# Kernel tuning notes

Measured on AMD Instinct MI355X. Metric: run time of the kernel, lower is better.

## Reference

```python
import math
import jax, jax.numpy as jnp
import numpy as np

B, D, N, KP1 = 64, 128, 500000, 4096  # batch, input_size, output_size, K+1
MOMENTUM = 0.5


def setup_inputs() -> dict:
    key = jax.random.key(0)
    k0, k1, k2, k3, k4, k5 = jax.random.split(key, 6)
    stdv = 1.0 / math.sqrt(D / 3)
    image = jax.random.normal(k0, (B, D), jnp.float32)
    gene = jax.random.normal(k1, (B, D), jnp.float32)
    index = jax.random.randint(k2, (B,), 0, N, dtype=jnp.int32)
    idx = jax.random.randint(k3, (B, KP1), 0, N, dtype=jnp.int32)
    idx = idx.at[:, 0].set(index)  # positive sample in slot 0
    memory_image = jax.random.uniform(k4, (N, D), jnp.float32) * (2 * stdv) - stdv
    memory_gene = jax.random.uniform(k5, (N, D), jnp.float32) * (2 * stdv) - stdv
    return {"image": image, "gene": gene, "memory_image": memory_image,
            "memory_gene": memory_gene, "index": index, "idx": idx}


def _momentum_update(mem, x, index):
    # gather positive rows, momentum blend, L2 normalize, scatter back
    pos = mem[index] * MOMENTUM + x * (1.0 - MOMENTUM)          # [B, D]
    pos = pos / jnp.sqrt(jnp.sum(pos * pos, axis=1, keepdims=True))
    return mem.at[index].set(pos)


def reference(image, gene, memory_image, memory_gene, index, idx):
    # gathered bank rows are detached in the original (weights .detach())
    w_gene = jax.lax.stop_gradient(memory_gene[idx])    # [B, K+1, D]
    w_image = jax.lax.stop_gradient(memory_image[idx])  # [B, K+1, D]
    # bmm([B,K+1,D], [B,D,1]) -> scores [B, K+1]; use_softmax=False branch:
    # stabilized softmax over the K+1 candidates (no temperature division)
    out_image = jax.nn.softmax(jnp.einsum('bkd,bd->bk', w_gene, image), axis=1)
    out_gene = jax.nn.softmax(jnp.einsum('bkd,bd->bk', w_image, gene), axis=1)
    # no_grad momentum scatter-update of the banks
    new_mem_image = _momentum_update(memory_image, jax.lax.stop_gradient(image), index)
    new_mem_gene = _momentum_update(memory_gene, jax.lax.stop_gradient(gene), index)
    return out_image, out_gene, new_mem_image, new_mem_gene
```

## Files before the change

kernel.cpp:

```cpp
#include <hip/hip_runtime.h>
#include <math.h>

constexpr int Bb   = 64;
constexpr int Dd   = 128;
constexpr int KP1  = 4096;
constexpr int Nrow = 500000;
constexpr long NMEM = (long)Nrow * Dd;
constexpr int BK   = Bb * KP1;

constexpr int MSLOT = 16;
constexpr int NGROUP = 31250;
constexpr int GPB    = 15625;
constexpr int SGQ    = 8;
constexpr int NSG    = (NGROUP + SGQ - 1) / SGQ;
constexpr long WS_NEED = (long)Nrow * 4 * (1 + MSLOT);

typedef float f4 __attribute__((ext_vector_type(4)));

__device__ __forceinline__ float dot8(float4 a, float4 b, float4 x0, float4 x1) {
    return a.x*x0.x + a.y*x0.y + a.z*x0.z + a.w*x0.w
         + b.x*x1.x + b.y*x1.y + b.z*x1.z + b.w*x1.w;
}


__global__ __launch_bounds__(512) void zero_cnt(int* cnt) {
    int i = blockIdx.x * 512 + threadIdx.x;
    for (; i < Nrow; i += gridDim.x * 512) cnt[i] = 0;
}

__global__ __launch_bounds__(512) void build_inv(
    const int* __restrict__ idx, int* __restrict__ cnt, int* __restrict__ entries)
{
    const int j = blockIdx.x * 512 + threadIdx.x;
    const int r = idx[j];
    const int c = atomicAdd(&cnt[r], 1);
    if (c < MSLOT) entries[r * MSLOT + c] = j;
}

__global__ __launch_bounds__(512, 2) void copy_score(
    const float* __restrict__ image, const float* __restrict__ gene,
    const float* __restrict__ mem_image, const float* __restrict__ mem_gene,
    const int* __restrict__ cnt, const int* __restrict__ entries,
    float* __restrict__ out)
{
    const int tid  = threadIdx.x;
    const int half = tid >> 5;
    const int lane = tid & 31;

    __shared__ f4  lxi[2048];
    __shared__ f4  lxg[2048];
    __shared__ int scnt[256];
    __shared__ int se0[256];
    {
        const f4* gi = (const f4*)image;
        const f4* gg = (const f4*)gene;
        #pragma unroll
        for (int u = 0; u < 4; ++u) {
            lxi[u * 512 + tid] = gi[u * 512 + tid];
            lxg[u * 512 + tid] = gg[u * 512 + tid];
        }
    }
    __syncthreads();

    const f4* srcI = (const f4*)mem_image;
    const f4* srcG = (const f4*)mem_gene;
    f4* dst = (f4*)(out + 2 * BK);

    for (int G0 = blockIdx.x * SGQ; G0 < NGROUP; G0 += gridDim.x * SGQ) {
        const int gl = (NGROUP - G0 < SGQ) ? (NGROUP - G0) : SGQ;

        f4 v[16];
        #pragma unroll
        for (int q = 0; q < SGQ; ++q) {
            if (q < gl) {
                const int G = G0 + q;
                const f4* s = (G < GPB) ? srcI + (long)G * 1024
                                        : srcG + (long)(G - GPB) * 1024;
                v[2 * q]     = s[tid];
                v[2 * q + 1] = s[512 + tid];
            }
        }
        {
            const int slot = tid & 255;
            const int q    = slot >> 5;
            if (q < gl) {
                const int G   = G0 + q;
                const int row = ((G < GPB) ? G : G - GPB) * 32 + (slot & 31);
                if (tid < 256) scnt[slot] = cnt[row];
                else           se0[slot]  = entries[row * MSLOT];
            }
        }

        #pragma unroll
        for (int q = 0; q < SGQ; ++q) {
            if (q < gl) {
                const long dbase = (long)(G0 + q) * 1024;
                __builtin_nontemporal_store(v[2 * q],     dst + dbase + tid);
                __builtin_nontemporal_store(v[2 * q + 1], dst + dbase + 512 + tid);
            }
        }
        __syncthreads();

        #pragma unroll
        for (int q = 0; q < SGQ; ++q) {
            if (q < gl) {
                const int G     = G0 + q;
                const int bank  = (G >= GPB);
                const int rbase = (bank ? G - GPB : G) * 32;
                const f4* lx    = bank ? lxi : lxg;
                float* odir     = bank ? out : out + BK;
                #pragma unroll
                for (int s2 = 0; s2 < 2; ++s2) {
                    const int slot = q * 32 + s2 * 16 + half;
                    int n = scnt[slot];
                    if (n <= 0) continue;
                    n = (n < MSLOT) ? n : MSLOT;
                    const f4 rv = v[2 * q + s2];
                    int j = se0[slot];
                    for (int e = 0;;) {
                        const f4 xv = lx[(j >> 12) * 32 + lane];
                        float s = rv.x*xv.x + rv.y*xv.y + rv.z*xv.z + rv.w*xv.w;
                        s += __shfl_xor(s, 1);
                        s += __shfl_xor(s, 2);
                        s += __shfl_xor(s, 4);
                        s += __shfl_xor(s, 8);
                        s += __shfl_xor(s, 16);
                        if (lane == 0) odir[j] = s;
                        if (++e >= n) break;
                        j = entries[(rbase + s2 * 16 + half) * MSLOT + e];
                    }
                }
            }
        }
        __syncthreads();
    }
}

__global__ __launch_bounds__(512) void epilogue(
    const float* __restrict__ image, const float* __restrict__ gene,
    const float* __restrict__ mem_image, const float* __restrict__ mem_gene,
    const int* __restrict__ index, float* __restrict__ out)
{
    const int tid = threadIdx.x;

    if (blockIdx.x < 128) {
        f4* row = (f4*)(out + (long)blockIdx.x * KP1);
        __shared__ float red[8];

        f4 a = row[tid], b = row[tid + 512];
        float m = fmaxf(fmaxf(fmaxf(a.x, a.y), fmaxf(a.z, a.w)),
                        fmaxf(fmaxf(b.x, b.y), fmaxf(b.z, b.w)));
        #pragma unroll
        for (int off = 1; off < 64; off <<= 1) m = fmaxf(m, __shfl_xor(m, off));
        if ((tid & 63) == 0) red[tid >> 6] = m;
        __syncthreads();
        if (tid < 64) {
            float tv = (tid < 8) ? red[tid] : -INFINITY;
            #pragma unroll
            for (int off = 1; off < 8; off <<= 1) tv = fmaxf(tv, __shfl_xor(tv, off));
            if (tid == 0) red[0] = tv;
        }
        __syncthreads();
        m = red[0];
        __syncthreads();

        a.x = expf(a.x - m); a.y = expf(a.y - m); a.z = expf(a.z - m); a.w = expf(a.w - m);
        b.x = expf(b.x - m); b.y = expf(b.y - m); b.z = expf(b.z - m); b.w = expf(b.w - m);
        float sum = a.x + a.y + a.z + a.w + b.x + b.y + b.z + b.w;
        #pragma unroll
        for (int off = 1; off < 64; off <<= 1) sum += __shfl_xor(sum, off);
        if ((tid & 63) == 0) red[tid >> 6] = sum;
        __syncthreads();
        if (tid < 64) {
            float tv = (tid < 8) ? red[tid] : 0.f;
            #pragma unroll
            for (int off = 1; off < 8; off <<= 1) tv += __shfl_xor(tv, off);
            if (tid == 0) red[0] = tv;
        }
        __syncthreads();
        const float inv = 1.0f / red[0];
        a *= inv; b *= inv;
        row[tid] = a; row[tid + 512] = b;
        return;
    }

    const int task  = ((blockIdx.x - 128) << 2) | (tid >> 7);
    const int sub   = tid >> 7;
    const int d     = tid & 127;
    const int which = task >> 6;
    const int b     = task & 63;
    const float* mem = which ? mem_gene : mem_image;
    const float* x   = which ? gene : image;
    float* o = out + 2 * BK + (long)which * NMEM;

    const long row = index[b];
    float p = mem[row * Dd + d] * 0.5f + x[(long)b * Dd + d] * 0.5f;
    float ss = p * p;
    #pragma unroll
    for (int off = 1; off < 64; off <<= 1) ss += __shfl_xor(ss, off);
    __shared__ float r2[8];
    if ((tid & 63) == 0) r2[tid >> 6] = ss;
    __syncthreads();
    const float inv = 1.0f / sqrtf(r2[2 * sub] + r2[2 * sub + 1]);
    o[row * Dd + d] = p * inv;
}


constexpr long HALF_F4    = NMEM / 4;
constexpr int  CHUNK_F4   = 8192;
constexpr int  FULL_PER_B = 1953;
constexpr long TAIL_BASE  = (long)FULL_PER_B * CHUNK_F4;
constexpr int  CHUNKS_PER_BANK = FULL_PER_B + 1;
constexpr int  NCHUNK     = 2 * CHUNKS_PER_BANK;

__global__ __launch_bounds__(64) void zero_ctr(unsigned* ctr) {
    if (threadIdx.x == 0) *ctr = 0u;
}

__global__ __launch_bounds__(512, 2) void fused_scores_copy(
    const float* __restrict__ image, const float* __restrict__ gene,
    const float* __restrict__ mem_image, const float* __restrict__ mem_gene,
    const int* __restrict__ idx, float* __restrict__ out, unsigned* __restrict__ ctr)
{
    const int tid = threadIdx.x;

    if (blockIdx.x < 128) {
        const int b     = blockIdx.x >> 1;
        const int which = blockIdx.x & 1;
        const float* w = which ? mem_image : mem_gene;
        const float* x = which ? gene : image;
        float* o = out + (long)which * BK + (long)b * KP1;

        __shared__ int   sidx[KP1];
        __shared__ float sv[KP1];
        __shared__ float red[8];
        {
            const int4* s4 = (const int4*)(idx + (long)b * KP1);
            int4* d4 = (int4*)sidx;
            d4[tid]       = s4[tid];
            d4[tid + 512] = s4[tid + 512];
        }
        const int lg  = tid & 15;
        const int grp = tid >> 4;
        float4 x0 = *(const float4*)(x + b * Dd + lg * 8);
        float4 x1 = *(const float4*)(x + b * Dd + lg * 8 + 4);
        __syncthreads();

        for (int j = 0; j < 128; j += 4) {
            const int k0 = grp + (j + 0) * 32;
            const int k1 = grp + (j + 1) * 32;
            const int k2 = grp + (j + 2) * 32;
            const int k3 = grp + (j + 3) * 32;
            const float4* r0 = (const float4*)(w + (long)sidx[k0] * Dd + lg * 8);
            const float4* r1 = (const float4*)(w + (long)sidx[k1] * Dd + lg * 8);
            const float4* r2 = (const float4*)(w + (long)sidx[k2] * Dd + lg * 8);
            const float4* r3 = (const float4*)(w + (long)sidx[k3] * Dd + lg * 8);
            float4 a0 = r0[0], b0 = r0[1];
            float4 a1 = r1[0], b1 = r1[1];
            float4 a2 = r2[0], b2 = r2[1];
            float4 a3 = r3[0], b3 = r3[1];
            float d0 = dot8(a0, b0, x0, x1);
            float d1 = dot8(a1, b1, x0, x1);
            float d2 = dot8(a2, b2, x0, x1);
            float d3 = dot8(a3, b3, x0, x1);
            d0 += __shfl_xor(d0, 1); d1 += __shfl_xor(d1, 1);
            d2 += __shfl_xor(d2, 1); d3 += __shfl_xor(d3, 1);
            d0 += __shfl_xor(d0, 2); d1 += __shfl_xor(d1, 2);
            d2 += __shfl_xor(d2, 2); d3 += __shfl_xor(d3, 2);
            d0 += __shfl_xor(d0, 4); d1 += __shfl_xor(d1, 4);
            d2 += __shfl_xor(d2, 4); d3 += __shfl_xor(d3, 4);
            d0 += __shfl_xor(d0, 8); d1 += __shfl_xor(d1, 8);
            d2 += __shfl_xor(d2, 8); d3 += __shfl_xor(d3, 8);
            if (lg == 0) { sv[k0] = d0; sv[k1] = d1; sv[k2] = d2; sv[k3] = d3; }
        }
        __syncthreads();

        float m = fmaxf(sv[tid], sv[tid + 512]);
        m = fmaxf(m, fmaxf(sv[tid + 1024], sv[tid + 1536]));
        m = fmaxf(m, fmaxf(sv[tid + 2048], sv[tid + 2560]));
        m = fmaxf(m, fmaxf(sv[tid + 3072], sv[tid + 3584]));
        #pragma unroll
        for (int off = 1; off < 64; off <<= 1) m = fmaxf(m, __shfl_xor(m, off));
        if ((tid & 63) == 0) red[tid >> 6] = m;
        __syncthreads();
        if (tid < 64) {
            float tv = (tid < 8) ? red[tid] : -INFINITY;
            #pragma unroll
            for (int off = 1; off < 8; off <<= 1) tv = fmaxf(tv, __shfl_xor(tv, off));
            if (tid == 0) red[0] = tv;
        }
        __syncthreads();
        m = red[0];
        __syncthreads();

        float sum = 0.f;
        #pragma unroll
        for (int r = 0; r < 8; ++r) {
            int k = tid + r * 512;
            float e = expf(sv[k] - m);
            sv[k] = e;
            sum += e;
        }
        #pragma unroll
        for (int off = 1; off < 64; off <<= 1) sum += __shfl_xor(sum, off);
        if ((tid & 63) == 0) red[tid >> 6] = sum;
        __syncthreads();
        if (tid < 64) {
            float tv = (tid < 8) ? red[tid] : 0.f;
            #pragma unroll
            for (int off = 1; off < 8; off <<= 1) tv += __shfl_xor(tv, off);
            if (tid == 0) red[0] = tv;
        }
        __syncthreads();
        const float inv = 1.0f / red[0];
        #pragma unroll
        for (int r = 0; r < 8; ++r) { int k = tid + r * 512; o[k] = sv[k] * inv; }
    }

    const f4* srcI = (const f4*)mem_image;
    const f4* srcG = (const f4*)mem_gene;
    f4* dst = (f4*)(out + 2 * BK);

    __shared__ unsigned sc;
    for (;;) {
        if (tid == 0) sc = atomicAdd(ctr, 1u);
        __syncthreads();
        const unsigned c = sc;
        __syncthreads();
        if (c >= NCHUNK) break;
        const int  bank  = (c < CHUNKS_PER_BANK) ? 0 : 1;
        const int  local = bank ? (int)(c - CHUNKS_PER_BANK) : (int)c;
        const f4*  sbank = bank ? srcG : srcI;
        const long dbank = (long)bank * HALF_F4;
        if (local < FULL_PER_B) {
            const long base = (long)local * CHUNK_F4;
            f4 v[16];
            #pragma unroll
            for (int k = 0; k < 16; ++k) v[k] = sbank[base + k * 512 + tid];
            #pragma unroll
            for (int k = 0; k < 16; ++k)
                __builtin_nontemporal_store(v[k], dst + dbank + base + k * 512 + tid);
        } else {
            f4 v0 = sbank[TAIL_BASE + tid];
            f4 v1 = sbank[TAIL_BASE + 512 + tid];
            __builtin_nontemporal_store(v0, dst + dbank + TAIL_BASE + tid);
            __builtin_nontemporal_store(v1, dst + dbank + TAIL_BASE + 512 + tid);
        }
    }
}

__global__ __launch_bounds__(128) void momentum_update(
    const float* __restrict__ image, const float* __restrict__ gene,
    const float* __restrict__ mem_image, const float* __restrict__ mem_gene,
    const int* __restrict__ index, float* __restrict__ out)
{
    const int b     = blockIdx.x;
    const int which = blockIdx.y;
    const float* mem = which ? mem_gene : mem_image;
    const float* x   = which ? gene : image;
    float* o = out + 2 * BK + (long)which * NMEM;
    const long row = index[b];
    const int d = threadIdx.x;
    float p = mem[row * Dd + d] * 0.5f + x[(long)b * Dd + d] * 0.5f;
    float ss = p * p;
    #pragma unroll
    for (int off = 1; off < 64; off <<= 1) ss += __shfl_xor(ss, off);
    __shared__ float r2[2];
    if ((d & 63) == 0) r2[d >> 6] = ss;
    __syncthreads();
    const float inv = 1.0f / sqrtf(r2[0] + r2[1]);
    o[row * Dd + d] = p * inv;
}

extern "C" void kernel_launch(void* const* d_in, const int* in_sizes, int n_in,
                              void* d_out, int out_size, void* d_ws, size_t ws_size,
                              hipStream_t stream) {
    const float* image     = (const float*)d_in[0];
    const float* gene      = (const float*)d_in[1];
    const float* mem_image = (const float*)d_in[2];
    const float* mem_gene  = (const float*)d_in[3];
    const int*   index     = (const int*)d_in[4];
    const int*   idx       = (const int*)d_in[5];
    float* out = (float*)d_out;

    if ((long)ws_size >= WS_NEED) {
        int* cnt     = (int*)d_ws;
        int* entries = cnt + Nrow;
        zero_cnt<<<dim3(1024), 512, 0, stream>>>(cnt);
        build_inv<<<dim3(512), 512, 0, stream>>>(idx, cnt, entries);
        copy_score<<<dim3(1954), 512, 0, stream>>>(
            image, gene, mem_image, mem_gene, cnt, entries, out);
        epilogue<<<dim3(160), 512, 0, stream>>>(
            image, gene, mem_image, mem_gene, index, out);
    } else {
        unsigned* ctr = (unsigned*)d_ws;
        zero_ctr<<<dim3(1), 64, 0, stream>>>(ctr);
        fused_scores_copy<<<dim3(2048), 512, 0, stream>>>(
            image, gene, mem_image, mem_gene, idx, out, ctr);
        momentum_update<<<dim3(64, 2), 128, 0, stream>>>(
            image, gene, mem_image, mem_gene, index, out);
    }
}
```

Baseline: 229.1 us.

## Restructure inverted-index copy_score into per-wave group ranges with packed count/first-entry metadata

The inverted index now packs each row's count and first entry into one int2, with overflow entries stored separately, and is cleared with a memset instead of a zeroing kernel. copy_score launches 512 blocks, each fixed to one bank so only that bank's query vectors go into LDS. Each 64-lane wave processes a contiguous range of 32-row groups without block-level barriers. Score dots use 16-lane subgroups that re-read the row from global memory, likely from cache, which trades extra loads for removing __syncthreads and raising occupancy.

```diff
diff --git a/kernel.cpp b/kernel.cpp
--- a/kernel.cpp
+++ b/kernel.cpp
@@ -7,13 +7,15 @@
 constexpr int Nrow = 500000;
 constexpr long NMEM = (long)Nrow * Dd;
 constexpr int BK   = Bb * KP1;
-
-constexpr int MSLOT = 16;
-constexpr int NGROUP = 31250;
-constexpr int GPB    = 15625;
-constexpr int SGQ    = 8;
-constexpr int NSG    = (NGROUP + SGQ - 1) / SGQ;
-constexpr long WS_NEED = (long)Nrow * 4 * (1 + MSLOT);
+constexpr long HALF_F4 = NMEM / 4;
+
+constexpr int GPB  = 15625;
+constexpr int NBLK = 512;
+constexpr int NWB  = (NBLK / 2) * 8;
+constexpr int OVSLOT = 15;
+constexpr long META_B    = (long)Nrow * 8;
+constexpr long ENTRIES_B = (long)Nrow * OVSLOT * 4;
+constexpr long WS_NEED   = META_B + ENTRIES_B;
 
 typedef float f4 __attribute__((ext_vector_type(4)));
 
@@ -23,116 +25,83 @@
 }
 
 
-__global__ __launch_bounds__(512) void zero_cnt(int* cnt) {
-    int i = blockIdx.x * 512 + threadIdx.x;
-    for (; i < Nrow; i += gridDim.x * 512) cnt[i] = 0;
-}
-
 __global__ __launch_bounds__(512) void build_inv(
-    const int* __restrict__ idx, int* __restrict__ cnt, int* __restrict__ entries)
+    const int* __restrict__ idx, int2* __restrict__ meta, int* __restrict__ entries)
 {
     const int j = blockIdx.x * 512 + threadIdx.x;
     const int r = idx[j];
-    const int c = atomicAdd(&cnt[r], 1);
-    if (c < MSLOT) entries[r * MSLOT + c] = j;
-}
-
-__global__ __launch_bounds__(512, 2) void copy_score(
+    const int c = atomicAdd(&meta[r].x, 1);
+    if (c == 0) meta[r].y = j;
+    else if (c <= OVSLOT) entries[(long)r * OVSLOT + (c - 1)] = j;
+}
+
+__global__ __launch_bounds__(512, 4) void copy_score(
     const float* __restrict__ image, const float* __restrict__ gene,
     const float* __restrict__ mem_image, const float* __restrict__ mem_gene,
-    const int* __restrict__ cnt, const int* __restrict__ entries,
+    const int2* __restrict__ meta, const int* __restrict__ entries,
     float* __restrict__ out)
 {
     const int tid  = threadIdx.x;
-    const int half = tid >> 5;
-    const int lane = tid & 31;
-
-    __shared__ f4  lxi[2048];
-    __shared__ f4  lxg[2048];
-    __shared__ int scnt[256];
-    __shared__ int se0[256];
+    const int bank = blockIdx.x & 1;
+    const int wid  = tid >> 6;
+    const int lane = tid & 63;
+    const int lg   = lane & 15;
+    const int sgid = (lane >> 4) & 3;
+
+    __shared__ f4 lx[2048];
     {
-        const f4* gi = (const f4*)image;
-        const f4* gg = (const f4*)gene;
-        #pragma unroll
-        for (int u = 0; u < 4; ++u) {
-            lxi[u * 512 + tid] = gi[u * 512 + tid];
-            lxg[u * 512 + tid] = gg[u * 512 + tid];
-        }
+        const f4* gx = bank ? (const f4*)image : (const f4*)gene;
+        #pragma unroll
+        for (int u = 0; u < 4; ++u) lx[u * 512 + tid] = gx[u * 512 + tid];
     }
     __syncthreads();
 
-    const f4* srcI = (const f4*)mem_image;
-    const f4* srcG = (const f4*)mem_gene;
-    f4* dst = (f4*)(out + 2 * BK);
-
-    for (int G0 = blockIdx.x * SGQ; G0 < NGROUP; G0 += gridDim.x * SGQ) {
-        const int gl = (NGROUP - G0 < SGQ) ? (NGROUP - G0) : SGQ;
+    const f4* src = bank ? (const f4*)mem_gene : (const f4*)mem_image;
+    f4* dst = (f4*)(out + 2 * BK) + (bank ? HALF_F4 : 0);
+    float* odir = bank ? out : out + BK;
+
+    const int wb = (blockIdx.x >> 1) * 8 + wid;
+    const long gs = (long)wb * GPB / NWB;
+    const long ge = (long)(wb + 1) * GPB / NWB;
+
+    for (long g = gs; g < ge; ++g) {
+        const long fbase = g * 1024;
+        const int  grow0 = (int)g * 32;
 
         f4 v[16];
         #pragma unroll
-        for (int q = 0; q < SGQ; ++q) {
-            if (q < gl) {
-                const int G = G0 + q;
-                const f4* s = (G < GPB) ? srcI + (long)G * 1024
-                                        : srcG + (long)(G - GPB) * 1024;
-                v[2 * q]     = s[tid];
-                v[2 * q + 1] = s[512 + tid];
+        for (int t = 0; t < 16; ++t) v[t] = src[fbase + t * 64 + lane];
+        int2 mt = make_int2(0, 0);
+        if (lane < 32) mt = meta[grow0 + lane];
+        #pragma unroll
+        for (int t = 0; t < 16; ++t)
+            __builtin_nontemporal_store(v[t], dst + fbase + t * 64 + lane);
+
+        for (int i = 0; i < 8; ++i) {
+            const int rr = sgid + 4 * i;
+            const int n0 = __shfl(mt.x, rr);
+            const int j0 = __shfl(mt.y, rr);
+            if (n0 <= 0) continue;
+            const int n = (n0 <= OVSLOT + 1) ? n0 : OVSLOT + 1;
+            int j = j0;
+            const long rbase = (long)(grow0 + rr) * 32;
+            const f4 r0 = src[rbase + lg];
+            const f4 r1 = src[rbase + 16 + lg];
+            for (int e = 0;;) {
+                const int bq = j >> 12;
+                const f4 x0 = lx[bq * 32 + lg];
+                const f4 x1 = lx[bq * 32 + 16 + lg];
+                float s = r0.x*x0.x + r0.y*x0.y + r0.z*x0.z + r0.w*x0.w
+                        + r1.x*x1.x + r1.y*x1.y + r1.z*x1.z + r1.w*x1.w;
+                s += __shfl_xor(s, 1);
+                s += __shfl_xor(s, 2);
+                s += __shfl_xor(s, 4);
+                s += __shfl_xor(s, 8);
+                if (lg == 0) odir[j] = s;
+                if (++e >= n) break;
+                j = entries[(long)(grow0 + rr) * OVSLOT + (e - 1)];
             }
         }
-        {
-            const int slot = tid & 255;
-            const int q    = slot >> 5;
-            if (q < gl) {
-                const int G   = G0 + q;
-                const int row = ((G < GPB) ? G : G - GPB) * 32 + (slot & 31);
-                if (tid < 256) scnt[slot] = cnt[row];
-                else           se0[slot]  = entries[row * MSLOT];
-            }
-        }
-
-        #pragma unroll
-        for (int q = 0; q < SGQ; ++q) {
-            if (q < gl) {
-                const long dbase = (long)(G0 + q) * 1024;
-                __builtin_nontemporal_store(v[2 * q],     dst + dbase + tid);
-                __builtin_nontemporal_store(v[2 * q + 1], dst + dbase + 512 + tid);
-            }
-        }
-        __syncthreads();
-
-        #pragma unroll
-        for (int q = 0; q < SGQ; ++q) {
-            if (q < gl) {
-                const int G     = G0 + q;
-                const int bank  = (G >= GPB);
-                const int rbase = (bank ? G - GPB : G) * 32;
-                const f4* lx    = bank ? lxi : lxg;
-                float* odir     = bank ? out : out + BK;
-                #pragma unroll
-                for (int s2 = 0; s2 < 2; ++s2) {
-                    const int slot = q * 32 + s2 * 16 + half;
-                    int n = scnt[slot];
-                    if (n <= 0) continue;
-                    n = (n < MSLOT) ? n : MSLOT;
-                    const f4 rv = v[2 * q + s2];
-                    int j = se0[slot];
-                    for (int e = 0;;) {
-                        const f4 xv = lx[(j >> 12) * 32 + lane];
-                        float s = rv.x*xv.x + rv.y*xv.y + rv.z*xv.z + rv.w*xv.w;
-                        s += __shfl_xor(s, 1);
-                        s += __shfl_xor(s, 2);
-                        s += __shfl_xor(s, 4);
-                        s += __shfl_xor(s, 8);
-                        s += __shfl_xor(s, 16);
-                        if (lane == 0) odir[j] = s;
-                        if (++e >= n) break;
-                        j = entries[(rbase + s2 * 16 + half) * MSLOT + e];
-                    }
-                }
-            }
-        }
-        __syncthreads();
     }
 }
 
@@ -206,7 +175,6 @@
 }
 
 
-constexpr long HALF_F4    = NMEM / 4;
 constexpr int  CHUNK_F4   = 8192;
 constexpr int  FULL_PER_B = 1953;
 constexpr long TAIL_BASE  = (long)FULL_PER_B * CHUNK_F4;
@@ -384,12 +352,12 @@
     float* out = (float*)d_out;
 
     if ((long)ws_size >= WS_NEED) {
-        int* cnt     = (int*)d_ws;
-        int* entries = cnt + Nrow;
-        zero_cnt<<<dim3(1024), 512, 0, stream>>>(cnt);
-        build_inv<<<dim3(512), 512, 0, stream>>>(idx, cnt, entries);
-        copy_score<<<dim3(1954), 512, 0, stream>>>(
-            image, gene, mem_image, mem_gene, cnt, entries, out);
+        int2* meta   = (int2*)d_ws;
+        int* entries = (int*)((char*)d_ws + META_B);
+        hipMemsetAsync(meta, 0, META_B, stream);
+        build_inv<<<dim3(512), 512, 0, stream>>>(idx, meta, entries);
+        copy_score<<<dim3(NBLK), 512, 0, stream>>>(
+            image, gene, mem_image, mem_gene, meta, entries, out);
         epilogue<<<dim3(160), 512, 0, stream>>>(
             image, gene, mem_image, mem_gene, index, out);
     } else {
```

Result: slower. 247.1 us (+7.8%).
